# Optimization experiments

Measured on AMD Instinct MI355X. Metric: run time of the kernel, lower is better.

The kernel has to match this reference:

```python
import jax, jax.numpy as jnp
import numpy as np

CH = 512


def _maxpool2(t):
    # 2x2 max pool, stride 2, NCHW
    B, C, H, W = t.shape
    return t.reshape(B, C, H // 2, 2, W // 2, 2).max(axis=(3, 5))


def setup_inputs() -> dict:
    key = jax.random.key(0)
    ks = jax.random.split(key, 6)
    B, C, H, W = 8, CH, 64, 64
    x = jax.random.normal(ks[0], (B, C, H, W), dtype=jnp.float32)
    # 1x1 conv weights stored as [out_ch, in_ch]
    w_theta = jax.random.normal(ks[1], (C // 8, C), dtype=jnp.float32) * (1.0 / np.sqrt(C))
    w_phi = jax.random.normal(ks[2], (C // 8, C), dtype=jnp.float32) * (1.0 / np.sqrt(C))
    w_g = jax.random.normal(ks[3], (C // 2, C), dtype=jnp.float32) * (1.0 / np.sqrt(C))
    w_o = jax.random.normal(ks[4], (C, C // 2), dtype=jnp.float32) * (1.0 / np.sqrt(C // 2))
    # gamma is a learned scalar (init 0.0 in the original); use 0.5 so the
    # attention branch contributes to the output for testing purposes.
    gamma = jnp.float32(0.5)
    return {"x": x, "w_theta": w_theta, "w_phi": w_phi, "w_g": w_g, "w_o": w_o, "gamma": gamma}


def reference(x, w_theta, w_phi, w_g, w_o, gamma):
    B, C, H, W = x.shape
    c8, c2 = C // 8, C // 2
    # 1x1 conv projections
    theta = jnp.einsum('bchw,oc->bohw', x, w_theta)           # [B, C/8, H, W]
    phi = _maxpool2(jnp.einsum('bchw,oc->bohw', x, w_phi))    # [B, C/8, H/2, W/2]
    g = _maxpool2(jnp.einsum('bchw,oc->bohw', x, w_g))        # [B, C/2, H/2, W/2]
    n, m = H * W, (H * W) // 4
    theta = theta.reshape(B, c8, n)
    phi = phi.reshape(B, c8, m)
    g = g.reshape(B, c2, m)
    # unscaled attention scores: [B, n, m]
    beta = jax.nn.softmax(jnp.einsum('bcn,bcm->bnm', theta, phi), axis=-1)
    # attend: g @ beta^T -> [B, C/2, n]
    att = jnp.einsum('bcm,bnm->bcn', g, beta).reshape(B, c2, H, W)
    o = jnp.einsum('bchw,oc->bohw', att, w_o)                 # [B, C, H, W]
    return gamma * o + x
```

## Files before the change

### kernel.cpp

```cpp
#include <hip/hip_runtime.h>
#include <math.h>

constexpr int CB = 8;
constexpr int CC = 512;
constexpr int CN = 4096;
constexpr int CM = 1024;
constexpr int C8 = 64;
constexpr int C2 = 256;

typedef __attribute__((ext_vector_type(8))) short short8;
typedef __attribute__((ext_vector_type(8))) _Float16 half8;
typedef __attribute__((ext_vector_type(4))) float f32x4;

__device__ inline unsigned short f2bf(float f) {
  unsigned int u = __float_as_uint(f);
  return (unsigned short)((u + 0x7FFFu + ((u >> 16) & 1u)) >> 16);
}
__device__ inline unsigned short f16bits(float f) {
  union { _Float16 h; unsigned short u; } c;
  c.h = (_Float16)f;
  return c.u;
}

__global__ __launch_bounds__(256)
void conv_w(const float* __restrict__ wt, const float* __restrict__ wp,
            const float* __restrict__ wg, const float* __restrict__ wo,
            _Float16* __restrict__ wth, _Float16* __restrict__ wtl,
            _Float16* __restrict__ wph, _Float16* __restrict__ wpl,
            _Float16* __restrict__ wgf, unsigned short* __restrict__ woh) {
  const int i = blockIdx.x * 256 + threadIdx.x;
  if (i < 32768) {
    float a = wt[i];
    _Float16 h = (_Float16)a;
    wth[i] = h; wtl[i] = (_Float16)(a - (float)h);
    a = wp[i];
    h = (_Float16)a;
    wph[i] = h; wpl[i] = (_Float16)(a - (float)h);
  }
  wgf[i] = (_Float16)wg[i];
  woh[i] = f2bf(wo[i]);
}

__global__ __launch_bounds__(256)
void xpose(const float* __restrict__ X, _Float16* __restrict__ xT) {
  __shared__ __align__(16) float raw[64][68];
  const int b = blockIdx.z, c0 = blockIdx.y * 64, n0 = blockIdx.x * 64;
  const float* Xb = X + ((size_t)b * CC + c0) * CN + n0;
  const int tid = threadIdx.x;
#pragma unroll
  for (int it = 0; it < 4; ++it) {
    const int idx = it * 256 + tid;
    const int row = idx >> 4, col4 = (idx & 15) * 4;
    *(float4*)&raw[row][col4] = *(const float4*)&Xb[(size_t)row * CN + col4];
  }
  __syncthreads();
  unsigned short* Yb = (unsigned short*)(xT + ((size_t)b * CN + n0) * CC + c0);
#pragma unroll
  for (int it = 0; it < 4; ++it) {
    const int idx = it * 256 + tid;
    const int n = idx >> 4, c4 = (idx & 15) * 4;
    ushort4 o;
    o.x = f16bits(raw[c4 + 0][n]);
    o.y = f16bits(raw[c4 + 1][n]);
    o.z = f16bits(raw[c4 + 2][n]);
    o.w = f16bits(raw[c4 + 3][n]);
    *(ushort4*)&Yb[(size_t)n * CC + c4] = o;
  }
}

__global__ __launch_bounds__(256)
void proj_th(const _Float16* __restrict__ Wh, const _Float16* __restrict__ Wl,
             const _Float16* __restrict__ xT, _Float16* __restrict__ thT) {
  __shared__ __align__(16) unsigned short LT[64][68];
  const int b = blockIdx.y, n0 = blockIdx.x * 64;
  const int tid = threadIdx.x;
  const int w = tid >> 6, l = tid & 63;
  const int l15 = l & 15, quad = l >> 4;
  f32x4 acc[4] = {};
  const _Float16* Brow = xT + (size_t)(b * CN + n0 + w * 16 + l15) * CC;
  for (int k0 = 0; k0 < CC; k0 += 32) {
    const half8 bfr = *(const half8*)&Brow[k0 + quad * 8];
#pragma unroll
    for (int i = 0; i < 4; ++i) {
      const half8 ah = *(const half8*)&Wh[(size_t)(i * 16 + l15) * CC + k0 + quad * 8];
      const half8 al = *(const half8*)&Wl[(size_t)(i * 16 + l15) * CC + k0 + quad * 8];
      acc[i] = __builtin_amdgcn_mfma_f32_16x16x32_f16(ah, bfr, acc[i], 0, 0, 0);
      acc[i] = __builtin_amdgcn_mfma_f32_16x16x32_f16(al, bfr, acc[i], 0, 0, 0);
    }
  }
#pragma unroll
  for (int i = 0; i < 4; ++i)
#pragma unroll
    for (int r = 0; r < 4; ++r)
      LT[w * 16 + l15][i * 16 + quad * 4 + r] = f16bits(acc[i][r]);
  __syncthreads();
  unsigned short* Yb = (unsigned short*)(thT + (size_t)(b * CN + n0) * C8);
#pragma unroll
  for (int it = 0; it < 4; ++it) {
    const int idx = it * 256 + tid;
    const int pos = idx >> 4, c4 = (idx & 15) * 4;
    ushort4 v = *(const ushort4*)&LT[pos][c4];
    *(ushort4*)&Yb[(size_t)pos * C8 + c4] = v;
  }
}

__global__ __launch_bounds__(256)
void proj_pg(const _Float16* __restrict__ Wph, const _Float16* __restrict__ Wpl,
             const _Float16* __restrict__ Wg, const _Float16* __restrict__ xT,
             _Float16* __restrict__ phT, unsigned short* __restrict__ gbf) {
  __shared__ float Pbuf[2][64][33];
  const int b = blockIdx.z, mt = blockIdx.y, tile = blockIdx.x;
  const int n0 = tile * 256;
  const int tid = threadIdx.x;
  const int w = tid >> 6, l = tid & 63;
  const int l15 = l & 15, quad = l >> 4;
  const bool isphi = (mt == 0);
  const _Float16* Ah = isphi ? Wph : (Wg + (size_t)(mt - 1) * 64 * CC);
  f32x4 acc[4][4] = {};
  const _Float16* Bbase = xT + (size_t)(b * CN + n0 + w * 64) * CC;
  for (int k0 = 0; k0 < CC; k0 += 32) {
    half8 bf[4], ah[4];
#pragma unroll
    for (int j = 0; j < 4; ++j)
      bf[j] = *(const half8*)&Bbase[(size_t)(j * 16 + l15) * CC + k0 + quad * 8];
#pragma unroll
    for (int i = 0; i < 4; ++i)
      ah[i] = *(const half8*)&Ah[(size_t)(i * 16 + l15) * CC + k0 + quad * 8];
#pragma unroll
    for (int i = 0; i < 4; ++i)
#pragma unroll
      for (int j = 0; j < 4; ++j)
        acc[i][j] = __builtin_amdgcn_mfma_f32_16x16x32_f16(ah[i], bf[j], acc[i][j], 0, 0, 0);
    if (isphi) {
      half8 al[4];
#pragma unroll
      for (int i = 0; i < 4; ++i)
        al[i] = *(const half8*)&Wpl[(size_t)(i * 16 + l15) * CC + k0 + quad * 8];
#pragma unroll
      for (int i = 0; i < 4; ++i)
#pragma unroll
        for (int j = 0; j < 4; ++j)
          acc[i][j] = __builtin_amdgcn_mfma_f32_16x16x32_f16(al[i], bf[j], acc[i][j], 0, 0, 0);
    }
  }
  const bool owner = ((l15 & 1) == 0);
  const int colh = l15 >> 1;
  if (w & 1) {
#pragma unroll
    for (int i = 0; i < 4; ++i)
#pragma unroll
      for (int j = 0; j < 4; ++j)
#pragma unroll
        for (int r = 0; r < 4; ++r) {
          float v = acc[i][j][r];
          float o = __shfl_xor(v, 1);
          v = fmaxf(v, o);
          if (owner) Pbuf[w >> 1][i * 16 + quad * 4 + r][j * 8 + colh] = v;
        }
  }
  __syncthreads();
  if (!(w & 1)) {
    const int pr = tile * 2 + (w >> 1);
    unsigned short* phB = (unsigned short*)(phT + ((size_t)b * CM + pr * 32) * C8);
#pragma unroll
    for (int i = 0; i < 4; ++i)
#pragma unroll
      for (int j = 0; j < 4; ++j)
#pragma unroll
        for (int r = 0; r < 4; ++r) {
          float v = acc[i][j][r];
          float o = __shfl_xor(v, 1);
          v = fmaxf(v, o);
          if (owner) {
            const int oc = i * 16 + quad * 4 + r;
            const int col = j * 8 + colh;
            v = fmaxf(v, Pbuf[w >> 1][oc][col]);
            if (isphi)
              phB[(size_t)col * C8 + oc] = f16bits(v);
            else
              gbf[((size_t)b * C2 + (mt - 1) * 64 + oc) * CM + pr * 32 + col] = f2bf(v);
          }
        }
  }
}

__global__ __launch_bounds__(256)
void attn_v4(const _Float16* __restrict__ thT, const _Float16* __restrict__ phT,
             const unsigned short* __restrict__ gbf,
             unsigned short* __restrict__ attbf) {
  __shared__ __align__(16) unsigned short Pl[2][4][16][40];
  __shared__ float Dinv[64];
  const int b = blockIdx.y;
  const int q0 = blockIdx.x * 64;
  const int tid = threadIdx.x;
  const int w = tid >> 6, l = tid & 63;
  const int l15 = l & 15, quad = l >> 4;
  half8 tb[2];
#pragma unroll
  for (int kc = 0; kc < 2; ++kc)
    tb[kc] = *(const half8*)&thT[(size_t)(b * CN + q0 + w * 16 + l15) * C8 +
                                 kc * 32 + quad * 8];
  f32x4 acc[4][4] = {};
  float dnp = 0.f;
  const _Float16* phB = phT + (size_t)b * CM * C8;
  const unsigned short* gB = gbf + (size_t)b * C2 * CM;

  for (int j0 = 0; j0 < CM; j0 += 32) {
    const int buf = (j0 >> 5) & 1;
    short8 gf[4];
#pragma unroll
    for (int ct = 0; ct < 4; ++ct)
      gf[ct] = *(const short8*)&gB[(size_t)(w * 64 + ct * 16 + l15) * CM +
                                   j0 + quad * 8];
    half8 pa[2][2];
#pragma unroll
    for (int jt = 0; jt < 2; ++jt)
#pragma unroll
      for (int kc = 0; kc < 2; ++kc)
        pa[jt][kc] = *(const half8*)&phB[(size_t)(j0 + jt * 16 + l15) * C8 +
                                         kc * 32 + quad * 8];
    f32x4 S0 = {0.f, 0.f, 0.f, 0.f}, S1 = {0.f, 0.f, 0.f, 0.f};
    S0 = __builtin_amdgcn_mfma_f32_16x16x32_f16(pa[0][0], tb[0], S0, 0, 0, 0);
    S0 = __builtin_amdgcn_mfma_f32_16x16x32_f16(pa[0][1], tb[1], S0, 0, 0, 0);
    S1 = __builtin_amdgcn_mfma_f32_16x16x32_f16(pa[1][0], tb[0], S1, 0, 0, 0);
    S1 = __builtin_amdgcn_mfma_f32_16x16x32_f16(pa[1][1], tb[1], S1, 0, 0, 0);
    float e0[4], e1[4];
#pragma unroll
    for (int r = 0; r < 4; ++r) { e0[r] = __expf(S0[r]); e1[r] = __expf(S1[r]); }
    dnp += (e0[0] + e0[1]) + (e0[2] + e0[3]) +
           (e1[0] + e1[1]) + (e1[2] + e1[3]);
    ushort4 w0, w1;
    w0.x = f2bf(e0[0]); w0.y = f2bf(e0[1]); w0.z = f2bf(e0[2]); w0.w = f2bf(e0[3]);
    w1.x = f2bf(e1[0]); w1.y = f2bf(e1[1]); w1.z = f2bf(e1[2]); w1.w = f2bf(e1[3]);
    *(ushort4*)&Pl[buf][w][l15][quad * 4] = w0;
    *(ushort4*)&Pl[buf][w][l15][16 + quad * 4] = w1;
    __syncthreads();
    short8 pfrag[4];
#pragma unroll
    for (int qs = 0; qs < 4; ++qs)
      pfrag[qs] = *(const short8*)&Pl[buf][qs][l15][quad * 8];
#pragma unroll
    for (int ct = 0; ct < 4; ++ct)
#pragma unroll
      for (int qs = 0; qs < 4; ++qs)
        acc[qs][ct] = __builtin_amdgcn_mfma_f32_16x16x32_bf16(pfrag[qs], gf[ct],
                                                              acc[qs][ct], 0, 0, 0);
  }
  float d = dnp;
  d += __shfl_xor(d, 16);
  d += __shfl_xor(d, 32);
  if (quad == 0) Dinv[w * 16 + l15] = 1.0f / d;
  __syncthreads();
  unsigned short* attB = attbf + (size_t)(b * CN + q0) * C2;
#pragma unroll
  for (int qs = 0; qs < 4; ++qs) {
#pragma unroll
    for (int r = 0; r < 4; ++r) {
      const int row = qs * 16 + quad * 4 + r;
      const float iv = Dinv[row];
#pragma unroll
      for (int ct = 0; ct < 4; ++ct)
        attB[(size_t)row * C2 + w * 64 + ct * 16 + l15] =
            f2bf(acc[qs][ct][r] * iv);
    }
  }
}

__global__ __launch_bounds__(256, 8)
void oproj_v2(const unsigned short* __restrict__ woh,
              const unsigned short* __restrict__ attbf,
              const float* __restrict__ X, const float* __restrict__ gamma,
              float* __restrict__ out) {
  __shared__ __align__(16) float Tw[4][16][34];
  const int b = blockIdx.z;
  const int mt = blockIdx.y;
  const int n0 = blockIdx.x * 64;
  const int tid = threadIdx.x;
  const int w = tid >> 6, l = tid & 63;
  const int l15 = l & 15, quad = l >> 4;
  const int wc = w >> 1, wn = w & 1;
  const int cbase = mt * 64 + wc * 32;
  const int nbase = n0 + wn * 32;
  const unsigned short* Bb = attbf + (size_t)b * CN * C2;
  f32x4 acc[2][2] = {};
  for (int k0 = 0; k0 < C2; k0 += 32) {
    short8 a[2], bb[2];
#pragma unroll
    for (int i = 0; i < 2; ++i)
      a[i] = *(const short8*)&woh[(size_t)(cbase + i * 16 + l15) * C2 + k0 + quad * 8];
#pragma unroll
    for (int j = 0; j < 2; ++j)
      bb[j] = *(const short8*)&Bb[(size_t)(nbase + j * 16 + l15) * C2 + k0 + quad * 8];
#pragma unroll
    for (int i = 0; i < 2; ++i)
#pragma unroll
      for (int j = 0; j < 2; ++j)
        acc[i][j] = __builtin_amdgcn_mfma_f32_16x16x32_bf16(a[i], bb[j], acc[i][j], 0, 0, 0);
  }
  const float gm = gamma[0];
  const int cp = l >> 2;
  const int nq = (l & 3) * 8;
#pragma unroll
  for (int i = 0; i < 2; ++i) {
#pragma unroll
    for (int j = 0; j < 2; ++j)
#pragma unroll
      for (int r = 0; r < 4; ++r)
        Tw[w][quad * 4 + r][j * 16 + l15] = acc[i][j][r];
    const float4 v0 = *(const float4*)&Tw[w][cp][nq];
    const float4 v1 = *(const float4*)&Tw[w][cp][nq + 4];
    const int c = cbase + i * 16 + cp;
    const size_t idx = ((size_t)b * CC + c) * CN + nbase + nq;
    const float4 x0 = *(const float4*)&X[idx];
    const float4 x1 = *(const float4*)&X[idx + 4];
    float4 o0, o1;
    o0.x = x0.x + gm * v0.x; o0.y = x0.y + gm * v0.y;
    o0.z = x0.z + gm * v0.z; o0.w = x0.w + gm * v0.w;
    o1.x = x1.x + gm * v1.x; o1.y = x1.y + gm * v1.y;
    o1.z = x1.z + gm * v1.z; o1.w = x1.w + gm * v1.w;
    *(float4*)&out[idx] = o0;
    *(float4*)&out[idx + 4] = o1;
    __syncthreads();
  }
}

extern "C" void kernel_launch(void* const* d_in, const int* in_sizes, int n_in,
                              void* d_out, int out_size, void* d_ws, size_t ws_size,
                              hipStream_t stream) {
  const float* x       = (const float*)d_in[0];
  const float* w_theta = (const float*)d_in[1];
  const float* w_phi   = (const float*)d_in[2];
  const float* w_g     = (const float*)d_in[3];
  const float* w_o     = (const float*)d_in[4];
  const float* gamma   = (const float*)d_in[5];
  float* out = (float*)d_out;
  char* wsb = (char*)d_ws;

  _Float16*       xT    = (_Float16*)(wsb + 0);
  _Float16*       thT   = (_Float16*)(wsb + 33554432);
  _Float16*       phT   = (_Float16*)(wsb + 37748736);
  unsigned short* gbf   = (unsigned short*)(wsb + 38797312);
  _Float16*       wth   = (_Float16*)(wsb + 42991616);
  _Float16*       wtl   = (_Float16*)(wsb + 43057152);
  _Float16*       wph   = (_Float16*)(wsb + 43122688);
  _Float16*       wpl   = (_Float16*)(wsb + 43188224);
  _Float16*       wgf   = (_Float16*)(wsb + 43253760);
  unsigned short* woh   = (unsigned short*)(wsb + 43515904);
  unsigned short* attbf = (unsigned short*)(wsb + 0);

  dim3 blk(256);
  conv_w<<<512, blk, 0, stream>>>(w_theta, w_phi, w_g, w_o,
                                  wth, wtl, wph, wpl, wgf, woh);
  xpose<<<dim3(64, 8, CB), blk, 0, stream>>>(x, xT);
  proj_th<<<dim3(64, CB), blk, 0, stream>>>(wth, wtl, xT, thT);
  proj_pg<<<dim3(16, 5, CB), blk, 0, stream>>>(wph, wpl, wgf, xT, phT, gbf);
  attn_v4<<<dim3(64, CB), blk, 0, stream>>>(thT, phT, gbf, attbf);
  oproj_v2<<<dim3(64, 8, CB), blk, 0, stream>>>(woh, attbf, x, gamma, out);
}
```

Before: 338.5 us.

## Halve attention query tile to double grid, preload all K-fragments in output projection

The attention kernel now handles 32 queries per block instead of 64, which doubles the grid from 512 to 1024 blocks. Each wave computes one 16x16 score tile (query-half by key-half) instead of two, and the two per-half partial softmax denominators are summed through shared memory. This should improve occupancy and load balance on a GPU with many CUs, at the cost of reloading the g fragments for twice as many blocks. The output projection loads all eight K-slices of both operands into registers up front, writes both accumulator tiles to shared memory at once and drops the per-iteration barrier, raising register pressure in exchange for more memory-level parallelism.

After: 367.8 us. 1.09x slower.

```diff
diff --git a/kernel.cpp b/kernel.cpp
--- a/kernel.cpp
+++ b/kernel.cpp
@@ -184,23 +184,24 @@
   }
 }
 
-__global__ __launch_bounds__(256)
-void attn_v4(const _Float16* __restrict__ thT, const _Float16* __restrict__ phT,
+__global__ __launch_bounds__(256, 4)
+void attn_v5(const _Float16* __restrict__ thT, const _Float16* __restrict__ phT,
              const unsigned short* __restrict__ gbf,
              unsigned short* __restrict__ attbf) {
-  __shared__ __align__(16) unsigned short Pl[2][4][16][40];
-  __shared__ float Dinv[64];
+  __shared__ __align__(16) unsigned short Pl[2][2][16][40];
+  __shared__ float Dpart[2][32];
   const int b = blockIdx.y;
-  const int q0 = blockIdx.x * 64;
+  const int q0 = blockIdx.x * 32;
   const int tid = threadIdx.x;
   const int w = tid >> 6, l = tid & 63;
   const int l15 = l & 15, quad = l >> 4;
+  const int qs = w & 1, jt = w >> 1;
   half8 tb[2];
 #pragma unroll
   for (int kc = 0; kc < 2; ++kc)
-    tb[kc] = *(const half8*)&thT[(size_t)(b * CN + q0 + w * 16 + l15) * C8 +
+    tb[kc] = *(const half8*)&thT[(size_t)(b * CN + q0 + qs * 16 + l15) * C8 +
                                  kc * 32 + quad * 8];
-  f32x4 acc[4][4] = {};
+  f32x4 acc[2][4] = {};
   float dnp = 0.f;
   const _Float16* phB = phT + (size_t)b * CM * C8;
   const unsigned short* gB = gbf + (size_t)b * C2 * CM;
@@ -212,66 +213,59 @@
     for (int ct = 0; ct < 4; ++ct)
       gf[ct] = *(const short8*)&gB[(size_t)(w * 64 + ct * 16 + l15) * CM +
                                    j0 + quad * 8];
-    half8 pa[2][2];
-#pragma unroll
-    for (int jt = 0; jt < 2; ++jt)
-#pragma unroll
-      for (int kc = 0; kc < 2; ++kc)
-        pa[jt][kc] = *(const half8*)&phB[(size_t)(j0 + jt * 16 + l15) * C8 +
-                                         kc * 32 + quad * 8];
-    f32x4 S0 = {0.f, 0.f, 0.f, 0.f}, S1 = {0.f, 0.f, 0.f, 0.f};
-    S0 = __builtin_amdgcn_mfma_f32_16x16x32_f16(pa[0][0], tb[0], S0, 0, 0, 0);
-    S0 = __builtin_amdgcn_mfma_f32_16x16x32_f16(pa[0][1], tb[1], S0, 0, 0, 0);
-    S1 = __builtin_amdgcn_mfma_f32_16x16x32_f16(pa[1][0], tb[0], S1, 0, 0, 0);
-    S1 = __builtin_amdgcn_mfma_f32_16x16x32_f16(pa[1][1], tb[1], S1, 0, 0, 0);
-    float e0[4], e1[4];
-#pragma unroll
-    for (int r = 0; r < 4; ++r) { e0[r] = __expf(S0[r]); e1[r] = __expf(S1[r]); }
-    dnp += (e0[0] + e0[1]) + (e0[2] + e0[3]) +
-           (e1[0] + e1[1]) + (e1[2] + e1[3]);
-    ushort4 w0, w1;
-    w0.x = f2bf(e0[0]); w0.y = f2bf(e0[1]); w0.z = f2bf(e0[2]); w0.w = f2bf(e0[3]);
-    w1.x = f2bf(e1[0]); w1.y = f2bf(e1[1]); w1.z = f2bf(e1[2]); w1.w = f2bf(e1[3]);
-    *(ushort4*)&Pl[buf][w][l15][quad * 4] = w0;
-    *(ushort4*)&Pl[buf][w][l15][16 + quad * 4] = w1;
+    half8 pa[2];
+#pragma unroll
+    for (int kc = 0; kc < 2; ++kc)
+      pa[kc] = *(const half8*)&phB[(size_t)(j0 + jt * 16 + l15) * C8 +
+                                   kc * 32 + quad * 8];
+    f32x4 S = {0.f, 0.f, 0.f, 0.f};
+    S = __builtin_amdgcn_mfma_f32_16x16x32_f16(pa[0], tb[0], S, 0, 0, 0);
+    S = __builtin_amdgcn_mfma_f32_16x16x32_f16(pa[1], tb[1], S, 0, 0, 0);
+    float e[4];
+#pragma unroll
+    for (int r = 0; r < 4; ++r) e[r] = __expf(S[r]);
+    dnp += (e[0] + e[1]) + (e[2] + e[3]);
+    ushort4 w0;
+    w0.x = f2bf(e[0]); w0.y = f2bf(e[1]); w0.z = f2bf(e[2]); w0.w = f2bf(e[3]);
+    *(ushort4*)&Pl[buf][qs][l15][jt * 16 + quad * 4] = w0;
     __syncthreads();
-    short8 pfrag[4];
-#pragma unroll
-    for (int qs = 0; qs < 4; ++qs)
-      pfrag[qs] = *(const short8*)&Pl[buf][qs][l15][quad * 8];
+    short8 pfrag[2];
+#pragma unroll
+    for (int q2 = 0; q2 < 2; ++q2)
+      pfrag[q2] = *(const short8*)&Pl[buf][q2][l15][quad * 8];
 #pragma unroll
     for (int ct = 0; ct < 4; ++ct)
 #pragma unroll
-      for (int qs = 0; qs < 4; ++qs)
-        acc[qs][ct] = __builtin_amdgcn_mfma_f32_16x16x32_bf16(pfrag[qs], gf[ct],
-                                                              acc[qs][ct], 0, 0, 0);
+      for (int q2 = 0; q2 < 2; ++q2)
+        acc[q2][ct] = __builtin_amdgcn_mfma_f32_16x16x32_bf16(pfrag[q2], gf[ct],
+                                                              acc[q2][ct], 0, 0, 0);
   }
   float d = dnp;
   d += __shfl_xor(d, 16);
   d += __shfl_xor(d, 32);
-  if (quad == 0) Dinv[w * 16 + l15] = 1.0f / d;
+  if (quad == 0) Dpart[jt][qs * 16 + l15] = d;
   __syncthreads();
   unsigned short* attB = attbf + (size_t)(b * CN + q0) * C2;
 #pragma unroll
-  for (int qs = 0; qs < 4; ++qs) {
+  for (int q2 = 0; q2 < 2; ++q2) {
 #pragma unroll
     for (int r = 0; r < 4; ++r) {
-      const int row = qs * 16 + quad * 4 + r;
-      const float iv = Dinv[row];
+      const int row = q2 * 16 + quad * 4 + r;
+      const float iv = 1.0f / (Dpart[0][row] + Dpart[1][row]);
 #pragma unroll
       for (int ct = 0; ct < 4; ++ct)
         attB[(size_t)row * C2 + w * 64 + ct * 16 + l15] =
-            f2bf(acc[qs][ct][r] * iv);
+            f2bf(acc[q2][ct][r] * iv);
     }
   }
 }
 
-__global__ __launch_bounds__(256, 8)
-void oproj_v2(const unsigned short* __restrict__ woh,
+__global__ __launch_bounds__(256, 3)
+void oproj_v3(const unsigned short* __restrict__ woh,
               const unsigned short* __restrict__ attbf,
               const float* __restrict__ X, const float* __restrict__ gamma,
               float* __restrict__ out) {
-  __shared__ __align__(16) float Tw[4][16][34];
+  __shared__ __align__(16) float Tw[2][4][16][34];
   const int b = blockIdx.z;
   const int mt = blockIdx.y;
   const int n0 = blockIdx.x * 64;
@@ -282,33 +276,41 @@
   const int cbase = mt * 64 + wc * 32;
   const int nbase = n0 + wn * 32;
   const unsigned short* Bb = attbf + (size_t)b * CN * C2;
+  short8 a[8][2], bb[8][2];
+#pragma unroll
+  for (int ks = 0; ks < 8; ++ks) {
+#pragma unroll
+    for (int i = 0; i < 2; ++i)
+      a[ks][i] = *(const short8*)&woh[(size_t)(cbase + i * 16 + l15) * C2 +
+                                      ks * 32 + quad * 8];
+#pragma unroll
+    for (int j = 0; j < 2; ++j)
+      bb[ks][j] = *(const short8*)&Bb[(size_t)(nbase + j * 16 + l15) * C2 +
+                                      ks * 32 + quad * 8];
+  }
   f32x4 acc[2][2] = {};
-  for (int k0 = 0; k0 < C2; k0 += 32) {
-    short8 a[2], bb[2];
+#pragma unroll
+  for (int ks = 0; ks < 8; ++ks)
 #pragma unroll
     for (int i = 0; i < 2; ++i)
-      a[i] = *(const short8*)&woh[(size_t)(cbase + i * 16 + l15) * C2 + k0 + quad * 8];
-#pragma unroll
-    for (int j = 0; j < 2; ++j)
-      bb[j] = *(const short8*)&Bb[(size_t)(nbase + j * 16 + l15) * C2 + k0 + quad * 8];
-#pragma unroll
-    for (int i = 0; i < 2; ++i)
 #pragma unroll
       for (int j = 0; j < 2; ++j)
-        acc[i][j] = __builtin_amdgcn_mfma_f32_16x16x32_bf16(a[i], bb[j], acc[i][j], 0, 0, 0);
-  }
+        acc[i][j] = __builtin_amdgcn_mfma_f32_16x16x32_bf16(a[ks][i], bb[ks][j],
+                                                            acc[i][j], 0, 0, 0);
   const float gm = gamma[0];
   const int cp = l >> 2;
   const int nq = (l & 3) * 8;
 #pragma unroll
+  for (int i = 0; i < 2; ++i)
+#pragma unroll
+    for (int j = 0; j < 2; ++j)
+#pragma unroll
+      for (int r = 0; r < 4; ++r)
+        Tw[i][w][quad * 4 + r][j * 16 + l15] = acc[i][j][r];
+#pragma unroll
   for (int i = 0; i < 2; ++i) {
-#pragma unroll
-    for (int j = 0; j < 2; ++j)
-#pragma unroll
-      for (int r = 0; r < 4; ++r)
-        Tw[w][quad * 4 + r][j * 16 + l15] = acc[i][j][r];
-    const float4 v0 = *(const float4*)&Tw[w][cp][nq];
-    const float4 v1 = *(const float4*)&Tw[w][cp][nq + 4];
+    const float4 v0 = *(const float4*)&Tw[i][w][cp][nq];
+    const float4 v1 = *(const float4*)&Tw[i][w][cp][nq + 4];
     const int c = cbase + i * 16 + cp;
     const size_t idx = ((size_t)b * CC + c) * CN + nbase + nq;
     const float4 x0 = *(const float4*)&X[idx];
@@ -320,7 +322,6 @@
     o1.z = x1.z + gm * v1.z; o1.w = x1.w + gm * v1.w;
     *(float4*)&out[idx] = o0;
     *(float4*)&out[idx + 4] = o1;
-    __syncthreads();
   }
 }
 
@@ -354,6 +355,6 @@
   xpose<<<dim3(64, 8, CB), blk, 0, stream>>>(x, xT);
   proj_th<<<dim3(64, CB), blk, 0, stream>>>(wth, wtl, xT, thT);
   proj_pg<<<dim3(16, 5, CB), blk, 0, stream>>>(wph, wpl, wgf, xT, phT, gbf);
-  attn_v4<<<dim3(64, CB), blk, 0, stream>>>(thT, phT, gbf, attbf);
-  oproj_v2<<<dim3(64, 8, CB), blk, 0, stream>>>(woh, attbf, x, gamma, out);
-}
+  attn_v5<<<dim3(128, CB), blk, 0, stream>>>(thT, phT, gbf, attbf);
+  oproj_v3<<<dim3(64, 8, CB), blk, 0, stream>>>(woh, attbf, x, gamma, out);
+}
```
